# Kernel optimization log

Hardware: AMD Instinct MI355X
Metric: run time of the kernel (lower is better)

Reference implementation:

```python
import jax, jax.numpy as jnp
import numpy as np
from jax.ops import segment_sum

N_NODES = 10000
N_EDGES = 160000
IN_FEAT = 256
OUT_FEAT = 256
NUM_RELS = 16


def setup_inputs() -> dict:
    key = jax.random.key(0)
    ks = jax.random.split(key, 8)
    feat = jax.random.normal(ks[0], (N_NODES, IN_FEAT), dtype=jnp.float32)
    Wf = jax.random.normal(ks[1], (NUM_RELS, IN_FEAT, OUT_FEAT), dtype=jnp.float32)
    Wb = jax.random.normal(ks[2], (NUM_RELS, IN_FEAT, OUT_FEAT), dtype=jnp.float32)
    loop_weight = jax.random.normal(ks[3], (IN_FEAT, OUT_FEAT), dtype=jnp.float32)
    forward_bias = jnp.zeros((OUT_FEAT,), dtype=jnp.float32)
    backward_bias = jnp.zeros((OUT_FEAT,), dtype=jnp.float32)
    self_bias = jnp.zeros((OUT_FEAT,), dtype=jnp.float32)
    src = jax.random.randint(ks[4], (N_EDGES,), 0, N_NODES, dtype=jnp.int32)
    dst = jax.random.randint(ks[5], (N_EDGES,), 0, N_NODES, dtype=jnp.int32)
    etypes = jax.random.randint(ks[6], (N_EDGES,), 0, NUM_RELS, dtype=jnp.int32)
    return {
        "feat": feat, "Wf": Wf, "Wb": Wb, "loop_weight": loop_weight,
        "forward_bias": forward_bias, "backward_bias": backward_bias,
        "self_bias": self_bias, "src": src, "dst": dst, "etypes": etypes,
        "use_dis_weight": 0, "drop_out": 0,
    }


def _inv_degree(idx, n):
    # dgl.norm_by_dst: 1/in-degree, with inf (zero-degree) replaced by 0
    deg = segment_sum(jnp.ones(idx.shape[0], dtype=jnp.float32), idx, num_segments=n)
    return jnp.where(deg > 0, 1.0 / deg, 0.0)


def _typed_pass(feat, W, bias, src_idx, dst_idx, etypes, norm_per_edge, n):
    # Per-relation projection of all nodes (grouped GEMM as R dense GEMMs),
    # then gather per-edge by (etype, src) -- avoids [E,in,out] weight gather.
    proj = jnp.einsum('ni,rio->rno', feat, W)          # [R, N, out]
    m = proj[etypes, src_idx] + bias                   # [E, out]
    m = m * norm_per_edge[:, None]
    return segment_sum(m, dst_idx, num_segments=n)     # [N, out]


def reference(feat, Wf, Wb, loop_weight, forward_bias, backward_bias,
              self_bias, src, dst, etypes, use_dis_weight, drop_out):
    n = feat.shape[0]
    # forward graph: messages src -> dst, norm by dst in-degree
    norm_f = _inv_degree(dst, n)[dst]                  # [E]
    m_forward = _typed_pass(feat, Wf, forward_bias, src, dst, etypes, norm_f, n)
    # reversed graph: src'=dst, dst'=src, same etype; norm by reversed dst in-degree
    norm_b = _inv_degree(src, n)[src]                  # [E]
    m_backward = _typed_pass(feat, Wb, backward_bias, dst, src, etypes, norm_b, n)
    # self loop (drop_out=False); faithful quirk: s += s + self_bias -> 2s + bias
    s = feat @ loop_weight
    s = s + s + self_bias
    return s + m_forward + m_backward
```

## Files before the change

kernel.cpp:

```cpp
#include <hip/hip_runtime.h>
#include <hip/hip_bf16.h>
#include <stdint.h>

#define N_NODES 10000
#define N_EDGES 160000
#define FEAT    256
#define NRELS   16
#define BM      64
#define NPROJ   33
#define GRIDX   40
#define KBYTES  512

typedef __attribute__((ext_vector_type(8))) short bf16x8;
typedef __attribute__((ext_vector_type(4))) float f32x4;

__device__ __forceinline__ unsigned short f2bf(float f) {
    union { float f; unsigned u; } v; v.f = f;
    unsigned u = v.u;
    u += 0x7FFFu + ((u >> 16) & 1u);
    return (unsigned short)(u >> 16);
}
__device__ __forceinline__ float bf2f(unsigned short u) {
    union { unsigned u; float f; } v; v.u = ((unsigned)u) << 16;
    return v.f;
}

__global__ __launch_bounds__(256) void k_prep(const float4* __restrict__ src4,
                                              ushort4* __restrict__ dst4, int n4,
                                              const int* __restrict__ src,
                                              const int* __restrict__ dst,
                                              int* degd, int* degs) {
    int i = blockIdx.x * 256 + threadIdx.x;
    if (i < n4) {
        float4 v = src4[i];
        ushort4 r;
        r.x = f2bf(v.x); r.y = f2bf(v.y); r.z = f2bf(v.z); r.w = f2bf(v.w);
        dst4[i] = r;
    }
    if (i < N_EDGES) {
        atomicAdd(&degd[dst[i]], 1);
        atomicAdd(&degs[src[i]], 1);
    }
}

__global__ __launch_bounds__(256) void k_wtall(const float* __restrict__ Wf,
                                               const float* __restrict__ Wb,
                                               const float* __restrict__ lw,
                                               unsigned short* __restrict__ wall) {
    __shared__ float tile[64][65];
    int z = blockIdx.z;
    const float* w;
    unsigned short* o;
    if (z < 16)      { w = Wf + (size_t)z * 65536;        o = wall + (size_t)(z * 2) * 65536; }
    else if (z < 32) { w = Wb + (size_t)(z - 16) * 65536; o = wall + (size_t)((z - 16) * 2 + 1) * 65536; }
    else             { w = lw;                            o = wall + (size_t)32 * 65536; }
    int i0 = blockIdx.x * 64, o0 = blockIdx.y * 64;
    int t = threadIdx.x;
    int c = t & 63, q = t >> 6;
#pragma unroll
    for (int it = 0; it < 16; it++) {
        int i = it * 4 + q;
        tile[i][c] = w[(size_t)(i0 + i) * 256 + o0 + c];
    }
    __syncthreads();
#pragma unroll
    for (int it = 0; it < 16; it++) {
        int oo = it * 4 + q;
        o[(size_t)(o0 + oo) * 256 + i0 + c] = f2bf(tile[c][oo]);
    }
}

__global__ __launch_bounds__(256) void k_off(const int* __restrict__ degd,
                                             const int* __restrict__ degs,
                                             int* offf, int* offb,
                                             int* curf, int* curb,
                                             float* normf, float* normb,
                                             int* gcnt) {
    __shared__ int sf[256], sb[256];
    __shared__ int basef, baseb;
    int t = threadIdx.x;
    int n = blockIdx.x * 256 + t;
    int df = (n < N_NODES) ? degd[n] : 0;
    int db = (n < N_NODES) ? degs[n] : 0;
    sf[t] = df; sb[t] = db;
    __syncthreads();
    for (int d = 1; d < 256; d <<= 1) {
        int vf = (t >= d) ? sf[t - d] : 0;
        int vb = (t >= d) ? sb[t - d] : 0;
        __syncthreads();
        sf[t] += vf; sb[t] += vb;
        __syncthreads();
    }
    if (t == 255) {
        basef = atomicAdd(&gcnt[0], sf[255]);
        baseb = atomicAdd(&gcnt[1], sb[255]);
    }
    __syncthreads();
    if (n < N_NODES) {
        int ef = basef + sf[t] - df;
        int eb = baseb + sb[t] - db;
        offf[n] = ef; offb[n] = eb;
        curf[n] = ef; curb[n] = eb;
        normf[n] = df > 0 ? 1.f / (float)df : 0.f;
        normb[n] = db > 0 ? 1.f / (float)db : 0.f;
    }
}

__global__ __launch_bounds__(256) void k_fill(const int* __restrict__ et,
                                              const int* __restrict__ src,
                                              const int* __restrict__ dst,
                                              int* curf, int* curb,
                                              int* csrf, int* csrb) {
    int e = blockIdx.x * 256 + threadIdx.x;
    if (e < N_EDGES) {
        int s = src[e], d = dst[e], r = et[e];
        csrf[atomicAdd(&curf[d], 1)] = (r * 2) * N_NODES + s;
        csrb[atomicAdd(&curb[s], 1)] = (r * 2 + 1) * N_NODES + d;
    }
}

__global__ __launch_bounds__(256) void k_proj(const unsigned short* __restrict__ featb,
                                              const unsigned short* __restrict__ wall,
                                              unsigned short* __restrict__ proj) {
    __shared__ __align__(16) char lds[BM * KBYTES];
    int rd = blockIdx.x;
    if (rd >= NPROJ) return;
    int m0 = blockIdx.y * BM;
    int t = threadIdx.x;
    int wave = t >> 6, lane = t & 63;
    int nb = wave * 64, lr = lane & 15, lg = lane >> 4;
    const unsigned short* wr = wall + (size_t)rd * 256 * FEAT;

    {
        int rl = t >> 5;
        int kb = (t & 31) << 4;
#pragma unroll
        for (int it = 0; it < 8; it++) {
            int row = it * 8 + rl;
            int gr = m0 + row; if (gr > N_NODES - 1) gr = N_NODES - 1;
            bf16x8 v = *(const bf16x8*)(featb + gr * FEAT + (kb >> 1));
            *(bf16x8*)(lds + row * KBYTES + (kb ^ ((row & 7) << 4))) = v;
        }
    }
    __syncthreads();

    f32x4 acc[4][4] = {};
#pragma unroll 2
    for (int k0 = 0; k0 < FEAT; k0 += 32) {
        int kb = (k0 + lg * 8) * 2;
        bf16x8 a[4], b[4];
        for (int ni = 0; ni < 4; ni++)
            b[ni] = *(const bf16x8*)(wr + (nb + ni * 16 + lr) * FEAT + k0 + lg * 8);
        for (int mi = 0; mi < 4; mi++) {
            int row = mi * 16 + lr;
            a[mi] = *(const bf16x8*)(lds + row * KBYTES + (kb ^ ((row & 7) << 4)));
        }
        for (int mi = 0; mi < 4; mi++)
            for (int ni = 0; ni < 4; ni++)
                acc[mi][ni] = __builtin_amdgcn_mfma_f32_16x16x32_bf16(a[mi], b[ni], acc[mi][ni], 0, 0, 0);
    }

    __syncthreads();
    for (int mi = 0; mi < 4; mi++) {
#pragma unroll
        for (int j = 0; j < 4; j++) {
            int row = mi * 16 + lg * 4 + j;
            int sw = (row & 7) << 4;
            for (int ni = 0; ni < 4; ni++) {
                int cb = (nb + ni * 16 + lr) * 2;
                *(unsigned short*)(lds + row * KBYTES + (cb ^ sw)) = f2bf(acc[mi][ni][j]);
            }
        }
    }
    __syncthreads();

    {
        int rl = t >> 5;
        int kb = (t & 31) << 4;
#pragma unroll
        for (int it = 0; it < 8; it++) {
            int row = it * 8 + rl;
            int gr = m0 + row;
            if (gr < N_NODES)
                *(bf16x8*)(proj + ((size_t)rd * N_NODES + gr) * FEAT + (kb >> 1)) =
                    *(const bf16x8*)(lds + row * KBYTES + (kb ^ ((row & 7) << 4)));
        }
    }
}

__global__ __launch_bounds__(256) void k_reduce(const unsigned short* __restrict__ proj,
                                                const int* __restrict__ csrf,
                                                const int* __restrict__ csrb,
                                                const int* __restrict__ offf,
                                                const int* __restrict__ offb,
                                                const int* __restrict__ degd,
                                                const int* __restrict__ degs,
                                                const float* __restrict__ normf,
                                                const float* __restrict__ normb,
                                                const float* __restrict__ biasf,
                                                const float* __restrict__ biasb,
                                                const float* __restrict__ sbias,
                                                float* __restrict__ out) {
    int node = blockIdx.x * 4 + (threadIdx.x >> 6);
    if (node >= N_NODES) return;
    int lane = threadIdx.x & 63;
    int half = lane >> 5;
    int li = lane & 31;

    float af[8] = {0,0,0,0,0,0,0,0};
    float ab[8] = {0,0,0,0,0,0,0,0};

    int b0 = offf[node], dfc = degd[node];
    int b1 = b0 + dfc;
#pragma unroll 4
    for (int s = b0 + half; s < b1; s += 2) {
        int c = csrf[s];
        bf16x8 m = *(const bf16x8*)(proj + (size_t)c * FEAT + li * 8);
#pragma unroll
        for (int k = 0; k < 8; k++) af[k] += bf2f((unsigned short)m[k]);
    }
    int c0 = offb[node], dbc = degs[node];
    int c1 = c0 + dbc;
#pragma unroll 4
    for (int s = c0 + half; s < c1; s += 2) {
        int c = csrb[s];
        bf16x8 m = *(const bf16x8*)(proj + (size_t)c * FEAT + li * 8);
#pragma unroll
        for (int k = 0; k < 8; k++) ab[k] += bf2f((unsigned short)m[k]);
    }

    float nf = normf[node], nbv = normb[node];
    float v[8];
#pragma unroll
    for (int k = 0; k < 8; k++) v[k] = nf * af[k] + nbv * ab[k];
#pragma unroll
    for (int k = 0; k < 8; k++) v[k] += __shfl_xor(v[k], 32);

    bf16x8 sf = *(const bf16x8*)(proj + ((size_t)32 * N_NODES + node) * FEAT + li * 8);

    int col = li * 8 + half * 4;
    float4 bfv = *(const float4*)(biasf + col);
    float4 bbv = *(const float4*)(biasb + col);
    float4 sbv = *(const float4*)(sbias + col);
    float fb = (dfc > 0) ? 1.f : 0.f;
    float bb = (dbc > 0) ? 1.f : 0.f;
    int k0 = half * 4;
    float4 o;
    o.x = v[k0 + 0] + 2.f * bf2f((unsigned short)sf[k0 + 0]) + sbv.x + fb * bfv.x + bb * bbv.x;
    o.y = v[k0 + 1] + 2.f * bf2f((unsigned short)sf[k0 + 1]) + sbv.y + fb * bfv.y + bb * bbv.y;
    o.z = v[k0 + 2] + 2.f * bf2f((unsigned short)sf[k0 + 2]) + sbv.z + fb * bfv.z + bb * bbv.z;
    o.w = v[k0 + 3] + 2.f * bf2f((unsigned short)sf[k0 + 3]) + sbv.w + fb * bfv.w + bb * bbv.w;
    *(float4*)(out + (size_t)node * FEAT + col) = o;
}

extern "C" void kernel_launch(void* const* d_in, const int* in_sizes, int n_in,
                              void* d_out, int out_size, void* d_ws, size_t ws_size,
                              hipStream_t stream) {
    const float* feat  = (const float*)d_in[0];
    const float* Wf    = (const float*)d_in[1];
    const float* Wb    = (const float*)d_in[2];
    const float* lw    = (const float*)d_in[3];
    const float* fbias = (const float*)d_in[4];
    const float* bbias = (const float*)d_in[5];
    const float* sbias = (const float*)d_in[6];
    const int*   src   = (const int*)d_in[7];
    const int*   dst   = (const int*)d_in[8];
    const int*   et    = (const int*)d_in[9];
    float* out = (float*)d_out;

    char* ws = (char*)d_ws;
    size_t off = 0;
    auto alloc = [&](size_t bytes) { void* p = ws + off; off = (off + bytes + 255) & ~(size_t)255; return p; };

    int*   degd  = (int*)alloc(N_NODES * 4);
    int*   degs  = (int*)alloc(N_NODES * 4);
    int*   gcnt  = (int*)alloc(64);
    size_t zero_bytes = off;
    int*   offf  = (int*)alloc(N_NODES * 4);
    int*   offb  = (int*)alloc(N_NODES * 4);
    int*   curf  = (int*)alloc(N_NODES * 4);
    int*   curb  = (int*)alloc(N_NODES * 4);
    float* normf = (float*)alloc(N_NODES * 4);
    float* normb = (float*)alloc(N_NODES * 4);
    int*   csrf  = (int*)alloc(N_EDGES * 4);
    int*   csrb  = (int*)alloc(N_EDGES * 4);
    unsigned short* featb = (unsigned short*)alloc((size_t)N_NODES * FEAT * 2);
    unsigned short* wall  = (unsigned short*)alloc((size_t)NPROJ * 256 * FEAT * 2);
    unsigned short* proj  = (unsigned short*)alloc((size_t)NPROJ * N_NODES * FEAT * 2);
    (void)ws_size;

    hipMemsetAsync(d_ws, 0, zero_bytes, stream);

    {
        int n4 = N_NODES * FEAT / 4;
        k_prep<<<(n4 + 255) / 256, 256, 0, stream>>>((const float4*)feat, (ushort4*)featb, n4,
                                                     src, dst, degd, degs);
    }
    {
        dim3 gw(4, 4, 33);
        k_wtall<<<gw, 256, 0, stream>>>(Wf, Wb, lw, wall);
    }
    k_off<<<(N_NODES + 255) / 256, 256, 0, stream>>>(degd, degs, offf, offb, curf, curb,
                                                     normf, normb, gcnt);
    k_fill<<<(N_EDGES + 255) / 256, 256, 0, stream>>>(et, src, dst, curf, curb, csrf, csrb);

    {
        dim3 grid(GRIDX, (N_NODES + BM - 1) / BM);
        k_proj<<<grid, 256, 0, stream>>>(featb, wall, proj);
    }

    k_reduce<<<(N_NODES + 3) / 4, 256, 0, stream>>>(proj, csrf, csrb, offf, offb,
                                                    degd, degs, normf, normb,
                                                    fbias, bbias, sbias, out);
}
```

Baseline: 204.1 us.

## Store projections node-major and compute self-loop GEMM in a separate kernel

The projection buffer is reorganised from relation-major to node-major ([node][32 chunks][256]), so the gathers in the reduction for a given source node hit nearby memory. The CSR entries are re-encoded to match the new layout. The self-loop projection moves out of the grouped GEMM into a new k_self kernel that writes fp32 2*s+bias straight into the output, which the reduction then read-modify-writes. The LDS swizzle on the epilogue store is also removed, which may add bank conflicts, and the extra output read/write adds traffic.

```diff
diff --git a/kernel.cpp b/kernel.cpp
--- a/kernel.cpp
+++ b/kernel.cpp
@@ -7,8 +7,7 @@
 #define FEAT    256
 #define NRELS   16
 #define BM      64
-#define NPROJ   33
-#define GRIDX   40
+#define NCHUNK  32
 #define KBYTES  512
 
 typedef __attribute__((ext_vector_type(8))) short bf16x8;
@@ -46,14 +45,15 @@
 __global__ __launch_bounds__(256) void k_wtall(const float* __restrict__ Wf,
                                                const float* __restrict__ Wb,
                                                const float* __restrict__ lw,
-                                               unsigned short* __restrict__ wall) {
+                                               unsigned short* __restrict__ wall,
+                                               unsigned short* __restrict__ lwt) {
     __shared__ float tile[64][65];
     int z = blockIdx.z;
     const float* w;
     unsigned short* o;
     if (z < 16)      { w = Wf + (size_t)z * 65536;        o = wall + (size_t)(z * 2) * 65536; }
     else if (z < 32) { w = Wb + (size_t)(z - 16) * 65536; o = wall + (size_t)((z - 16) * 2 + 1) * 65536; }
-    else             { w = lw;                            o = wall + (size_t)32 * 65536; }
+    else             { w = lw;                            o = lwt; }
     int i0 = blockIdx.x * 64, o0 = blockIdx.y * 64;
     int t = threadIdx.x;
     int c = t & 63, q = t >> 6;
@@ -114,8 +114,45 @@
     int e = blockIdx.x * 256 + threadIdx.x;
     if (e < N_EDGES) {
         int s = src[e], d = dst[e], r = et[e];
-        csrf[atomicAdd(&curf[d], 1)] = (r * 2) * N_NODES + s;
-        csrb[atomicAdd(&curb[s], 1)] = (r * 2 + 1) * N_NODES + d;
+        csrf[atomicAdd(&curf[d], 1)] = s * NCHUNK + r * 2;
+        csrb[atomicAdd(&curb[s], 1)] = d * NCHUNK + r * 2 + 1;
+    }
+}
+
+__global__ __launch_bounds__(256) void k_self(const unsigned short* __restrict__ featb,
+                                              const unsigned short* __restrict__ lwt,
+                                              const float* __restrict__ sbias,
+                                              float* __restrict__ out) {
+    int m0 = blockIdx.x * BM;
+    int wave = threadIdx.x >> 6, lane = threadIdx.x & 63;
+    int nb = wave * 64, lr = lane & 15, lg = lane >> 4;
+    f32x4 acc[4][4] = {};
+    for (int k0 = 0; k0 < FEAT; k0 += 32) {
+        int kk = k0 + lg * 8;
+        bf16x8 a[4], b[4];
+        for (int mi = 0; mi < 4; mi++) {
+            int row = m0 + mi * 16 + lr;
+            if (row >= N_NODES) row = N_NODES - 1;
+            a[mi] = *(const bf16x8*)(featb + row * FEAT + kk);
+        }
+        for (int ni = 0; ni < 4; ni++) {
+            int col = nb + ni * 16 + lr;
+            b[ni] = *(const bf16x8*)(lwt + col * FEAT + kk);
+        }
+        for (int mi = 0; mi < 4; mi++)
+            for (int ni = 0; ni < 4; ni++)
+                acc[mi][ni] = __builtin_amdgcn_mfma_f32_16x16x32_bf16(a[mi], b[ni], acc[mi][ni], 0, 0, 0);
+    }
+    for (int mi = 0; mi < 4; mi++) {
+        for (int j = 0; j < 4; j++) {
+            int row = m0 + mi * 16 + lg * 4 + j;
+            if (row < N_NODES) {
+                for (int ni = 0; ni < 4; ni++) {
+                    int col = nb + ni * 16 + lr;
+                    out[row * FEAT + col] = 2.0f * acc[mi][ni][j] + sbias[col];
+                }
+            }
+        }
     }
 }
 
@@ -124,7 +161,6 @@
                                               unsigned short* __restrict__ proj) {
     __shared__ __align__(16) char lds[BM * KBYTES];
     int rd = blockIdx.x;
-    if (rd >= NPROJ) return;
     int m0 = blockIdx.y * BM;
     int t = threadIdx.x;
     int wave = t >> 6, lane = t & 63;
@@ -159,17 +195,15 @@
             for (int ni = 0; ni < 4; ni++)
                 acc[mi][ni] = __builtin_amdgcn_mfma_f32_16x16x32_bf16(a[mi], b[ni], acc[mi][ni], 0, 0, 0);
     }
-
-    __syncthreads();
+    __syncthreads();
+
     for (int mi = 0; mi < 4; mi++) {
 #pragma unroll
         for (int j = 0; j < 4; j++) {
             int row = mi * 16 + lg * 4 + j;
-            int sw = (row & 7) << 4;
-            for (int ni = 0; ni < 4; ni++) {
-                int cb = (nb + ni * 16 + lr) * 2;
-                *(unsigned short*)(lds + row * KBYTES + (cb ^ sw)) = f2bf(acc[mi][ni][j]);
-            }
+            for (int ni = 0; ni < 4; ni++)
+                *(unsigned short*)(lds + row * KBYTES + (nb + ni * 16 + lr) * 2) =
+                    f2bf(acc[mi][ni][j]);
         }
     }
     __syncthreads();
@@ -182,8 +216,8 @@
             int row = it * 8 + rl;
             int gr = m0 + row;
             if (gr < N_NODES)
-                *(bf16x8*)(proj + ((size_t)rd * N_NODES + gr) * FEAT + (kb >> 1)) =
-                    *(const bf16x8*)(lds + row * KBYTES + (kb ^ ((row & 7) << 4)));
+                *(bf16x8*)(proj + ((size_t)gr * NCHUNK + rd) * FEAT + (kb >> 1)) =
+                    *(const bf16x8*)(lds + row * KBYTES + kb);
         }
     }
 }
@@ -199,7 +233,6 @@
                                                 const float* __restrict__ normb,
                                                 const float* __restrict__ biasf,
                                                 const float* __restrict__ biasb,
-                                                const float* __restrict__ sbias,
                                                 float* __restrict__ out) {
     int node = blockIdx.x * 4 + (threadIdx.x >> 6);
     if (node >= N_NODES) return;
@@ -236,20 +269,17 @@
 #pragma unroll
     for (int k = 0; k < 8; k++) v[k] += __shfl_xor(v[k], 32);
 
-    bf16x8 sf = *(const bf16x8*)(proj + ((size_t)32 * N_NODES + node) * FEAT + li * 8);
-
     int col = li * 8 + half * 4;
     float4 bfv = *(const float4*)(biasf + col);
     float4 bbv = *(const float4*)(biasb + col);
-    float4 sbv = *(const float4*)(sbias + col);
     float fb = (dfc > 0) ? 1.f : 0.f;
     float bb = (dbc > 0) ? 1.f : 0.f;
+    float4 o = *(float4*)(out + (size_t)node * FEAT + col);
     int k0 = half * 4;
-    float4 o;
-    o.x = v[k0 + 0] + 2.f * bf2f((unsigned short)sf[k0 + 0]) + sbv.x + fb * bfv.x + bb * bbv.x;
-    o.y = v[k0 + 1] + 2.f * bf2f((unsigned short)sf[k0 + 1]) + sbv.y + fb * bfv.y + bb * bbv.y;
-    o.z = v[k0 + 2] + 2.f * bf2f((unsigned short)sf[k0 + 2]) + sbv.z + fb * bfv.z + bb * bbv.z;
-    o.w = v[k0 + 3] + 2.f * bf2f((unsigned short)sf[k0 + 3]) + sbv.w + fb * bfv.w + bb * bbv.w;
+    o.x += v[k0 + 0] + fb * bfv.x + bb * bbv.x;
+    o.y += v[k0 + 1] + fb * bfv.y + bb * bbv.y;
+    o.z += v[k0 + 2] + fb * bfv.z + bb * bbv.z;
+    o.w += v[k0 + 3] + fb * bfv.w + bb * bbv.w;
     *(float4*)(out + (size_t)node * FEAT + col) = o;
 }
 
@@ -285,8 +315,9 @@
     int*   csrf  = (int*)alloc(N_EDGES * 4);
     int*   csrb  = (int*)alloc(N_EDGES * 4);
     unsigned short* featb = (unsigned short*)alloc((size_t)N_NODES * FEAT * 2);
-    unsigned short* wall  = (unsigned short*)alloc((size_t)NPROJ * 256 * FEAT * 2);
-    unsigned short* proj  = (unsigned short*)alloc((size_t)NPROJ * N_NODES * FEAT * 2);
+    unsigned short* wall  = (unsigned short*)alloc((size_t)NCHUNK * 256 * FEAT * 2);
+    unsigned short* lwt   = (unsigned short*)alloc((size_t)FEAT * FEAT * 2);
+    unsigned short* proj  = (unsigned short*)alloc((size_t)N_NODES * NCHUNK * FEAT * 2);
     (void)ws_size;
 
     hipMemsetAsync(d_ws, 0, zero_bytes, stream);
@@ -298,18 +329,20 @@
     }
     {
         dim3 gw(4, 4, 33);
-        k_wtall<<<gw, 256, 0, stream>>>(Wf, Wb, lw, wall);
+        k_wtall<<<gw, 256, 0, stream>>>(Wf, Wb, lw, wall, lwt);
     }
     k_off<<<(N_NODES + 255) / 256, 256, 0, stream>>>(degd, degs, offf, offb, curf, curb,
                                                      normf, normb, gcnt);
     k_fill<<<(N_EDGES + 255) / 256, 256, 0, stream>>>(et, src, dst, curf, curb, csrf, csrb);
 
-    {
-        dim3 grid(GRIDX, (N_NODES + BM - 1) / BM);
+    k_self<<<(N_NODES + BM - 1) / BM, 256, 0, stream>>>(featb, lwt, sbias, out);
+
+    {
+        dim3 grid(NCHUNK, (N_NODES + BM - 1) / BM);
         k_proj<<<grid, 256, 0, stream>>>(featb, wall, proj);
     }
 
     k_reduce<<<(N_NODES + 3) / 4, 256, 0, stream>>>(proj, csrf, csrb, offf, offb,
                                                     degd, degs, normf, normb,
-                                                    fbias, bbias, sbias, out);
-}
+                                                    fbias, bbias, out);
+}
```

Measured after the change: 187.9 us. -8.0%, faster.
